# Optimization experiments

Measured on AMD Instinct MI355X. Metric: run time of the kernel, lower is better.

Reference implementation:

```python
import jax, jax.numpy as jnp
import numpy as np

F = 1024      # features
CF = 768      # context_features
H = 8         # num_heads
D = 64        # head_features
MID = H * D   # 512
SCALE = D ** -0.5


def _ln(x, g, b):
    m = jnp.mean(x, axis=-1, keepdims=True)
    v = jnp.var(x, axis=-1, keepdims=True)
    return (x - m) / jnp.sqrt(v + 1e-5) * g + b


def _attention(x, ctx, ng, nb, ncg, ncb, wq, wkv, wo, bo):
    # pre-norms (Attention.forward)
    xn = _ln(x, ng, nb)
    cn = _ln(ctx, ncg, ncb)
    q = xn @ wq                              # [b, n, MID]
    k, v = jnp.split(cn @ wkv, 2, axis=-1)   # [b, m, MID] each
    b, n, _ = q.shape
    m = k.shape[1]
    q = q.reshape(b, n, H, D).transpose(0, 2, 1, 3)  # b h n d
    k = k.reshape(b, m, H, D).transpose(0, 2, 1, 3)
    v = v.reshape(b, m, H, D).transpose(0, 2, 1, 3)
    sim = jnp.einsum('bhnd,bhmd->bhnm', q, k) * SCALE   # use_rel_pos=False
    attn = jax.nn.softmax(sim, axis=-1)
    out = jnp.einsum('bhnm,bhmd->bhnd', attn, v)
    out = out.transpose(0, 2, 1, 3).reshape(b, n, MID)
    return out @ wo + bo


def setup_inputs() -> dict:
    key = jax.random.key(0)
    ks = jax.random.split(key, 16)
    s = 0.02
    inp = {
        'x': jax.random.normal(ks[0], (4, 2048, F), jnp.float32),
        'context': jax.random.normal(ks[1], (4, 512, CF), jnp.float32),
        # self-attention params
        'sa_ng': jnp.ones((F,), jnp.float32),
        'sa_nb': jnp.zeros((F,), jnp.float32),
        'sa_ncg': jnp.ones((F,), jnp.float32),
        'sa_ncb': jnp.zeros((F,), jnp.float32),
        'sa_wq': jax.random.normal(ks[2], (F, MID), jnp.float32) * s,
        'sa_wkv': jax.random.normal(ks[3], (F, 2 * MID), jnp.float32) * s,
        'sa_wo': jax.random.normal(ks[4], (MID, F), jnp.float32) * s,
        'sa_bo': jnp.zeros((F,), jnp.float32),
        # cross-attention params
        'ca_ng': jnp.ones((F,), jnp.float32),
        'ca_nb': jnp.zeros((F,), jnp.float32),
        'ca_ncg': jnp.ones((CF,), jnp.float32),
        'ca_ncb': jnp.zeros((CF,), jnp.float32),
        'ca_wq': jax.random.normal(ks[5], (F, MID), jnp.float32) * s,
        'ca_wkv': jax.random.normal(ks[6], (CF, 2 * MID), jnp.float32) * s,
        'ca_wo': jax.random.normal(ks[7], (MID, F), jnp.float32) * s,
        'ca_bo': jnp.zeros((F,), jnp.float32),
    }
    return inp


def reference(x, context,
              sa_ng, sa_nb, sa_ncg, sa_ncb, sa_wq, sa_wkv, sa_wo, sa_bo,
              ca_ng, ca_nb, ca_ncg, ca_ncb, ca_wq, ca_wkv, ca_wo, ca_bo):
    # AttentionBlock.forward: x = self_attn(x) + x; x = cross_attn(x, ctx) + x
    x = _attention(x, x, sa_ng, sa_nb, sa_ncg, sa_ncb, sa_wq, sa_wkv, sa_wo, sa_bo) + x
    x = _attention(x, context, ca_ng, ca_nb, ca_ncg, ca_ncb, ca_wq, ca_wkv, ca_wo, ca_bo) + x
    return x
```

## Files before the change

kernel.cpp:

```cpp
#include <hip/hip_runtime.h>
#include <hip/hip_bf16.h>

typedef __bf16 bf16x8 __attribute__((ext_vector_type(8)));
typedef float  f32x4  __attribute__((ext_vector_type(4)));

#define MFMA16(a, b, c) __builtin_amdgcn_mfma_f32_16x16x32_bf16((a), (b), (c), 0, 0, 0)

__device__ __forceinline__ void async16(void* lds, const void* g) {
    __builtin_amdgcn_global_load_lds(
        (const __attribute__((address_space(1))) unsigned int*)g,
        (__attribute__((address_space(3))) unsigned int*)lds, 16, 0, 0);
}

__global__ __launch_bounds__(256) void tconv_kernel(const float* __restrict__ W,
                                                    __bf16* __restrict__ WT,
                                                    int K, int N) {
    __shared__ __bf16 t[64][65];
    int n0 = blockIdx.x * 64, k0 = blockIdx.y * 64;
    int tx = threadIdx.x & 63, ty = threadIdx.x >> 6;
    for (int r = ty; r < 64; r += 4)
        t[r][tx] = (__bf16)W[(size_t)(k0 + r) * N + n0 + tx];
    __syncthreads();
    for (int rr = ty; rr < 64; rr += 4)
        WT[(size_t)(n0 + rr) * K + k0 + tx] = t[tx][rr];
}

template <int C>
__global__ __launch_bounds__(256) void ln_kernel(const float* __restrict__ x,
                                                 const float* __restrict__ g,
                                                 const float* __restrict__ b,
                                                 __bf16* __restrict__ out) {
    int row = blockIdx.x;
    const float* xr = x + (size_t)row * C;
    float s1 = 0.f, s2 = 0.f;
    float v[(C == 1024) ? 4 : 3];
    if constexpr (C == 1024) {
        float4 f = *(const float4*)&xr[threadIdx.x * 4];
        v[0] = f.x; v[1] = f.y; v[2] = f.z; v[3] = f.w;
#pragma unroll
        for (int i = 0; i < 4; i++) { s1 += v[i]; s2 += v[i] * v[i]; }
    } else {
#pragma unroll
        for (int i = 0; i < 3; i++) {
            v[i] = xr[threadIdx.x + i * 256];
            s1 += v[i]; s2 += v[i] * v[i];
        }
    }
#pragma unroll
    for (int off = 1; off < 64; off <<= 1) {
        s1 += __shfl_xor(s1, off);
        s2 += __shfl_xor(s2, off);
    }
    __shared__ float p1[4], p2[4];
    int wave = threadIdx.x >> 6;
    if ((threadIdx.x & 63) == 0) { p1[wave] = s1; p2[wave] = s2; }
    __syncthreads();
    s1 = p1[0] + p1[1] + p1[2] + p1[3];
    s2 = p2[0] + p2[1] + p2[2] + p2[3];
    float mean = s1 / C;
    float rstd = rsqrtf(s2 / C - mean * mean + 1e-5f);
    __bf16* orow = out + (size_t)row * C;
    if constexpr (C == 1024) {
        union { __bf16 h[4]; unsigned long long u; } pk;
#pragma unroll
        for (int i = 0; i < 4; i++) {
            int c = threadIdx.x * 4 + i;
            pk.h[i] = (__bf16)((v[i] - mean) * rstd * g[c] + b[c]);
        }
        *(unsigned long long*)&orow[threadIdx.x * 4] = pk.u;
    } else {
#pragma unroll
        for (int i = 0; i < 3; i++) {
            int c = threadIdx.x + i * 256;
            orow[c] = (__bf16)((v[i] - mean) * rstd * g[c] + b[c]);
        }
    }
}

__global__ __launch_bounds__(256) void ln2_kernel(const float* __restrict__ x,
                                                  const float* __restrict__ g1,
                                                  const float* __restrict__ b1,
                                                  const float* __restrict__ g2,
                                                  const float* __restrict__ b2,
                                                  __bf16* __restrict__ o1,
                                                  __bf16* __restrict__ o2) {
    constexpr int C = 1024;
    int row = blockIdx.x;
    const float* xr = x + (size_t)row * C;
    float4 f = *(const float4*)&xr[threadIdx.x * 4];
    float v[4] = {f.x, f.y, f.z, f.w};
    float s1 = 0.f, s2 = 0.f;
#pragma unroll
    for (int i = 0; i < 4; i++) { s1 += v[i]; s2 += v[i] * v[i]; }
#pragma unroll
    for (int off = 1; off < 64; off <<= 1) {
        s1 += __shfl_xor(s1, off);
        s2 += __shfl_xor(s2, off);
    }
    __shared__ float p1[4], p2[4];
    int wave = threadIdx.x >> 6;
    if ((threadIdx.x & 63) == 0) { p1[wave] = s1; p2[wave] = s2; }
    __syncthreads();
    s1 = p1[0] + p1[1] + p1[2] + p1[3];
    s2 = p2[0] + p2[1] + p2[2] + p2[3];
    float mean = s1 / C;
    float rstd = rsqrtf(s2 / C - mean * mean + 1e-5f);
    union { __bf16 h[4]; unsigned long long u; } pk1, pk2;
#pragma unroll
    for (int i = 0; i < 4; i++) {
        int c = threadIdx.x * 4 + i;
        float nv = (v[i] - mean) * rstd;
        pk1.h[i] = (__bf16)(nv * g1[c] + b1[c]);
        pk2.h[i] = (__bf16)(nv * g2[c] + b2[c]);
    }
    *(unsigned long long*)&o1[(size_t)row * C + threadIdx.x * 4] = pk1.u;
    *(unsigned long long*)&o2[(size_t)row * C + threadIdx.x * 4] = pk2.u;
}

template <int EPI>
__device__ __forceinline__ void gemm_core(const __bf16* __restrict__ A,
                                          const __bf16* __restrict__ BT,
                                          void* __restrict__ Cout,
                                          int N, int K, int bm, int bn,
                                          const float* __restrict__ bias,
                                          const float* __restrict__ res,
                                          __bf16* Al, __bf16* Bl) {
    int tid = threadIdx.x;
    int lane = tid & 63, wave = tid >> 6;
    int quad = lane >> 4, l15 = lane & 15;
    int wm = wave >> 1, wn = wave & 1;
    const __bf16* Ab = A + (size_t)(bm * 128) * K;
    const __bf16* Bb = BT + (size_t)(bn * 128) * K;
    f32x4 acc[4][4] = {};
    for (int k0 = 0; k0 < K; k0 += 32) {
#pragma unroll
        for (int j = 0; j < 2; j++) {
            int sbase = wave * 128 + j * 64;
            int s = sbase + lane;
            int r = s >> 2, c = (s & 3) ^ (r & 3);
            async16((char*)Al + sbase * 16, &Ab[(size_t)r * K + k0 + c * 8]);
            async16((char*)Bl + sbase * 16, &Bb[(size_t)r * K + k0 + c * 8]);
        }
        __syncthreads();
        bf16x8 a[4], b[4];
#pragma unroll
        for (int i = 0; i < 4; i++) {
            int row = wm * 64 + i * 16 + l15;
            a[i] = *(const bf16x8*)&Al[row * 32 + (quad ^ (row & 3)) * 8];
        }
#pragma unroll
        for (int t = 0; t < 4; t++) {
            int row = wn * 64 + t * 16 + l15;
            b[t] = *(const bf16x8*)&Bl[row * 32 + (quad ^ (row & 3)) * 8];
        }
#pragma unroll
        for (int i = 0; i < 4; i++)
#pragma unroll
            for (int t = 0; t < 4; t++) acc[i][t] = MFMA16(a[i], b[t], acc[i][t]);
        __syncthreads();
    }
#pragma unroll
    for (int i = 0; i < 4; i++) {
#pragma unroll
        for (int t = 0; t < 4; t++) {
#pragma unroll
            for (int r = 0; r < 4; r++) {
                int row = bm * 128 + wm * 64 + i * 16 + quad * 4 + r;
                int col = bn * 128 + wn * 64 + t * 16 + l15;
                float vv = acc[i][t][r];
                if (EPI == 0) {
                    ((__bf16*)Cout)[(size_t)row * N + col] = (__bf16)vv;
                } else {
                    ((float*)Cout)[(size_t)row * N + col] =
                        vv + bias[col] + res[(size_t)row * N + col];
                }
            }
        }
    }
}

template <int EPI>
__global__ __launch_bounds__(256) void gemm_bt(const __bf16* __restrict__ A,
                                               const __bf16* __restrict__ BT,
                                               void* __restrict__ Cout,
                                               int M, int N, int K,
                                               const float* __restrict__ bias,
                                               const float* __restrict__ res) {
    __shared__ __align__(16) __bf16 Al[128 * 32];
    __shared__ __align__(16) __bf16 Bl[128 * 32];
    gemm_core<EPI>(A, BT, Cout, N, K, blockIdx.x, blockIdx.y, bias, res, Al, Bl);
}

__global__ __launch_bounds__(256) void gemm_fused3(
    const __bf16* A0, const __bf16* B0, __bf16* C0, int N0, int K0, int nbn0,
    const __bf16* A1, const __bf16* B1, __bf16* C1, int N1, int K1, int nbn1,
    const __bf16* A2, const __bf16* B2, __bf16* C2, int N2, int K2, int nbn2,
    int c0, int c1) {
    __shared__ __align__(16) __bf16 Al[128 * 32];
    __shared__ __align__(16) __bf16 Bl[128 * 32];
    int id = blockIdx.x;
    if (id < c0) {
        gemm_core<0>(A0, B0, C0, N0, K0, id / nbn0, id % nbn0, nullptr, nullptr, Al, Bl);
    } else if (id < c1) {
        id -= c0;
        gemm_core<0>(A1, B1, C1, N1, K1, id / nbn1, id % nbn1, nullptr, nullptr, Al, Bl);
    } else {
        id -= c1;
        gemm_core<0>(A2, B2, C2, N2, K2, id / nbn2, id % nbn2, nullptr, nullptr, Al, Bl);
    }
}

__global__ __launch_bounds__(256) void flash_kernel(const __bf16* __restrict__ q,
                                                    const __bf16* __restrict__ kb,
                                                    const __bf16* __restrict__ vt,
                                                    __bf16* __restrict__ out,
                                                    int n, int m) {
    __shared__ __align__(16) __bf16 Qs[64 * 64];
    __shared__ __align__(16) __bf16 Ks[64 * 64];
    __shared__ __align__(16) __bf16 VTs[64 * 64];
    __shared__ __align__(16) __bf16 Ps[64 * 64];
    int tid = threadIdx.x;
    int lane = tid & 63, w = tid >> 6;
    int quad = lane >> 4, l15 = lane & 15;
    int qt = blockIdx.x, h = blockIdx.y, b = blockIdx.z;
    const size_t BM = (size_t)gridDim.z * m;
    const int qrow = w * 16 + l15;

#pragma unroll
    for (int j = 0; j < 2; j++) {
        int sbase = w * 128 + j * 64;
        int s = sbase + lane;
        int r = s >> 3, c = (s & 7) ^ (r & 7);
        async16((char*)Qs + sbase * 16,
                &q[(size_t)(b * n + qt * 64 + r) * 512 + h * 64 + c * 8]);
    }

    f32x4 acc[4] = {};
    float l_part = 0.f;

    int nkt = m / 64;
    for (int kt = 0; kt < nkt; kt++) {
#pragma unroll
        for (int j = 0; j < 2; j++) {
            int sbase = w * 128 + j * 64;
            int s = sbase + lane;
            int r = s >> 3, c = (s & 7) ^ (r & 7);
            async16((char*)Ks + sbase * 16,
                    &kb[(size_t)(b * m + kt * 64 + r) * 512 + h * 64 + c * 8]);
            async16((char*)VTs + sbase * 16,
                    &vt[(size_t)(h * 64 + r) * BM + b * m + kt * 64 + c * 8]);
        }
        __syncthreads();

        f32x4 sacc[4] = {};
#pragma unroll
        for (int kk = 0; kk < 64; kk += 32) {
            int jb = ((kk >> 3) + quad) ^ (qrow & 7);
            bf16x8 bq = *(const bf16x8*)&Qs[qrow * 64 + jb * 8];
#pragma unroll
            for (int t = 0; t < 4; t++) {
                int krow = t * 16 + l15;
                int ja = ((kk >> 3) + quad) ^ (krow & 7);
                bf16x8 ak = *(const bf16x8*)&Ks[krow * 64 + ja * 8];
                sacc[t] = MFMA16(ak, bq, sacc[t]);
            }
        }

#pragma unroll
        for (int t = 0; t < 4; t++) {
            float e0 = __expf(sacc[t][0] * 0.125f);
            float e1 = __expf(sacc[t][1] * 0.125f);
            float e2 = __expf(sacc[t][2] * 0.125f);
            float e3 = __expf(sacc[t][3] * 0.125f);
            l_part += (e0 + e1) + (e2 + e3);
            union { __bf16 h[4]; unsigned long long u; } pk;
            pk.h[0] = (__bf16)e0; pk.h[1] = (__bf16)e1;
            pk.h[2] = (__bf16)e2; pk.h[3] = (__bf16)e3;
            int chunk = t * 2 + (quad >> 1);
            int off = qrow * 64 + (chunk ^ (qrow & 7)) * 8 + (quad & 1) * 4;
            *(unsigned long long*)&Ps[off] = pk.u;
        }

#pragma unroll
        for (int kk = 0; kk < 64; kk += 32) {
            int jp = ((kk >> 3) + quad) ^ (qrow & 7);
            bf16x8 ap = *(const bf16x8*)&Ps[qrow * 64 + jp * 8];
#pragma unroll
            for (int t2 = 0; t2 < 4; t2++) {
                int drow = t2 * 16 + l15;
                int jv = ((kk >> 3) + quad) ^ (drow & 7);
                bf16x8 bv = *(const bf16x8*)&VTs[drow * 64 + jv * 8];
                acc[t2] = MFMA16(ap, bv, acc[t2]);
            }
        }
        __syncthreads();
    }

    l_part += __shfl_xor(l_part, 16);
    l_part += __shfl_xor(l_part, 32);
    float rinv = 1.0f / l_part;
#pragma unroll
    for (int r = 0; r < 4; r++) {
        float rl = __shfl(rinv, quad * 4 + r);
        int row = b * n + qt * 64 + w * 16 + quad * 4 + r;
#pragma unroll
        for (int t2 = 0; t2 < 4; t2++)
            out[(size_t)row * 512 + h * 64 + t2 * 16 + l15] =
                (__bf16)(acc[t2][r] * rl);
    }
}

extern "C" void kernel_launch(void* const* d_in, const int* in_sizes, int n_in,
                              void* d_out, int out_size, void* d_ws, size_t ws_size,
                              hipStream_t stream) {
    const float* x      = (const float*)d_in[0];
    const float* ctx    = (const float*)d_in[1];
    const float* sa_ng  = (const float*)d_in[2];
    const float* sa_nb  = (const float*)d_in[3];
    const float* sa_ncg = (const float*)d_in[4];
    const float* sa_ncb = (const float*)d_in[5];
    const float* sa_wq  = (const float*)d_in[6];
    const float* sa_wkv = (const float*)d_in[7];
    const float* sa_wo  = (const float*)d_in[8];
    const float* sa_bo  = (const float*)d_in[9];
    const float* ca_ng  = (const float*)d_in[10];
    const float* ca_nb  = (const float*)d_in[11];
    const float* ca_ncg = (const float*)d_in[12];
    const float* ca_ncb = (const float*)d_in[13];
    const float* ca_wq  = (const float*)d_in[14];
    const float* ca_wkv = (const float*)d_in[15];
    const float* ca_wo  = (const float*)d_in[16];
    const float* ca_bo  = (const float*)d_in[17];
    float* out = (float*)d_out;

    const int B = 4, N = 2048, M = 512, F = 1024, CF = 768, MID = 512;
    const int ROWS = B * N;
    const int CROWS = B * M;

    char* ws = (char*)d_ws;
    size_t off = 0;
    auto alloc = [&](size_t bytes) {
        void* p = ws + off;
        off = (off + bytes + 255) & ~(size_t)255;
        return p;
    };
    __bf16* wqT   = (__bf16*)alloc((size_t)MID * F * 2);
    __bf16* wkvT  = (__bf16*)alloc((size_t)(2 * MID) * F * 2);
    __bf16* woT   = (__bf16*)alloc((size_t)F * MID * 2);
    __bf16* cwqT  = (__bf16*)alloc((size_t)MID * F * 2);
    __bf16* cwkvT = (__bf16*)alloc((size_t)(2 * MID) * CF * 2);
    __bf16* cwoT  = (__bf16*)alloc((size_t)F * MID * 2);
    __bf16* xn1   = (__bf16*)alloc((size_t)ROWS * F * 2);
    __bf16* xn2   = (__bf16*)alloc((size_t)ROWS * F * 2);
    __bf16* qb    = (__bf16*)alloc((size_t)ROWS * MID * 2);
    __bf16* kb    = (__bf16*)alloc((size_t)ROWS * MID * 2);
    __bf16* vt    = (__bf16*)alloc((size_t)MID * ROWS * 2);
    __bf16* ao    = (__bf16*)alloc((size_t)ROWS * MID * 2);
    float*  x1    = (float*)alloc((size_t)ROWS * F * 4);
    (void)ws_size; (void)in_sizes; (void)n_in; (void)out_size;

    dim3 blk(256);

    tconv_kernel<<<dim3(MID / 64, F / 64), blk, 0, stream>>>(sa_wq, wqT, F, MID);
    tconv_kernel<<<dim3((2 * MID) / 64, F / 64), blk, 0, stream>>>(sa_wkv, wkvT, F, 2 * MID);
    tconv_kernel<<<dim3(F / 64, MID / 64), blk, 0, stream>>>(sa_wo, woT, MID, F);
    tconv_kernel<<<dim3(MID / 64, F / 64), blk, 0, stream>>>(ca_wq, cwqT, F, MID);
    tconv_kernel<<<dim3((2 * MID) / 64, CF / 64), blk, 0, stream>>>(ca_wkv, cwkvT, CF, 2 * MID);
    tconv_kernel<<<dim3(F / 64, MID / 64), blk, 0, stream>>>(ca_wo, cwoT, MID, F);

    ln2_kernel<<<dim3(ROWS), blk, 0, stream>>>(x, sa_ng, sa_nb, sa_ncg, sa_ncb, xn1, xn2);
    {
        int c0 = (ROWS / 128) * (MID / 128);
        int c1 = c0 + (ROWS / 128) * (MID / 128);
        int c2 = c1 + (MID / 128) * (ROWS / 128);
        gemm_fused3<<<dim3(c2), blk, 0, stream>>>(
            xn1, wqT, qb, MID, F, MID / 128,
            xn2, wkvT, kb, MID, F, MID / 128,
            wkvT + (size_t)MID * F, xn2, vt, ROWS, F, ROWS / 128,
            c0, c1);
    }
    flash_kernel<<<dim3(N / 64, 8, B), blk, 0, stream>>>(qb, kb, vt, ao, N, N);
    gemm_bt<1><<<dim3(ROWS / 128, F / 128), blk, 0, stream>>>(
        ao, woT, x1, ROWS, F, MID, sa_bo, x);

    ln_kernel<1024><<<dim3(ROWS), blk, 0, stream>>>(x1, ca_ng, ca_nb, xn1);
    ln_kernel<768><<<dim3(CROWS), blk, 0, stream>>>(ctx, ca_ncg, ca_ncb, xn2);
    {
        int c0 = (ROWS / 128) * (MID / 128);
        int c1 = c0 + (CROWS / 128) * (MID / 128);
        int c2 = c1 + (MID / 128) * (CROWS / 128);
        gemm_fused3<<<dim3(c2), blk, 0, stream>>>(
            xn1, cwqT, qb, MID, F, MID / 128,
            xn2, cwkvT, kb, MID, CF, MID / 128,
            cwkvT + (size_t)MID * CF, xn2, vt, CROWS, CF, CROWS / 128,
            c0, c1);
    }
    flash_kernel<<<dim3(N / 64, 8, B), blk, 0, stream>>>(qb, kb, vt, ao, N, M);
    gemm_bt<1><<<dim3(ROWS / 128, F / 128), blk, 0, stream>>>(
        ao, cwoT, out, ROWS, F, MID, ca_bo, x1);
}
```

Baseline: 355.4 us.

## Merge weight-transpose and LN launches, widen GEMM K-tile, fold softmax scale into Q

Merges the six weight-transpose launches into one kernel, and the two cross-attention layernorm launches into one. Doubles the GEMM K step to 64 with an 8-way XOR swizzle, halving the number of barrier pairs per tile. Folds the softmax scale and log2(e) into the Q projection epilogue so the flash kernel can use a raw exp2 builtin instead of a scaled expf. Rounding Q to bf16 after scaling changes numerics slightly, and the larger LDS tiles may lower occupancy.

```diff
diff --git a/kernel.cpp b/kernel.cpp
--- a/kernel.cpp
+++ b/kernel.cpp
@@ -5,6 +5,14 @@
 typedef float  f32x4  __attribute__((ext_vector_type(4)));
 
 #define MFMA16(a, b, c) __builtin_amdgcn_mfma_f32_16x16x32_bf16((a), (b), (c), 0, 0, 0)
+
+__device__ __forceinline__ float fast_exp2(float x) {
+#if __has_builtin(__builtin_amdgcn_exp2f)
+    return __builtin_amdgcn_exp2f(x);
+#else
+    return exp2f(x);
+#endif
+}
 
 __device__ __forceinline__ void async16(void* lds, const void* g) {
     __builtin_amdgcn_global_load_lds(
@@ -12,28 +20,43 @@
         (__attribute__((address_space(3))) unsigned int*)lds, 16, 0, 0);
 }
 
-__global__ __launch_bounds__(256) void tconv_kernel(const float* __restrict__ W,
-                                                    __bf16* __restrict__ WT,
-                                                    int K, int N) {
-    __shared__ __bf16 t[64][65];
-    int n0 = blockIdx.x * 64, k0 = blockIdx.y * 64;
+__device__ __forceinline__ void tconv_tile(const float* __restrict__ W,
+                                           __bf16* __restrict__ WT,
+                                           int K, int N, int id, int nbx,
+                                           __bf16 (*t)[65]) {
+    int n0 = (id % nbx) * 64, k0 = (id / nbx) * 64;
     int tx = threadIdx.x & 63, ty = threadIdx.x >> 6;
+#pragma unroll
     for (int r = ty; r < 64; r += 4)
         t[r][tx] = (__bf16)W[(size_t)(k0 + r) * N + n0 + tx];
     __syncthreads();
+#pragma unroll
     for (int rr = ty; rr < 64; rr += 4)
         WT[(size_t)(n0 + rr) * K + k0 + tx] = t[tx][rr];
 }
 
+__global__ __launch_bounds__(256) void tconv6_kernel(
+    const float* W0, __bf16* T0, const float* W1, __bf16* T1,
+    const float* W2, __bf16* T2, const float* W3, __bf16* T3,
+    const float* W4, __bf16* T4, const float* W5, __bf16* T5) {
+    __shared__ __bf16 t[64][65];
+    int id = blockIdx.x;
+    if (id < 128)      tconv_tile(W0, T0, 1024, 512,  id,       8,  t);
+    else if (id < 384) tconv_tile(W1, T1, 1024, 1024, id - 128, 16, t);
+    else if (id < 512) tconv_tile(W2, T2, 512,  1024, id - 384, 16, t);
+    else if (id < 640) tconv_tile(W3, T3, 1024, 512,  id - 512, 8,  t);
+    else if (id < 832) tconv_tile(W4, T4, 768,  1024, id - 640, 16, t);
+    else               tconv_tile(W5, T5, 512,  1024, id - 832, 16, t);
+}
+
 template <int C>
-__global__ __launch_bounds__(256) void ln_kernel(const float* __restrict__ x,
-                                                 const float* __restrict__ g,
-                                                 const float* __restrict__ b,
-                                                 __bf16* __restrict__ out) {
-    int row = blockIdx.x;
-    const float* xr = x + (size_t)row * C;
-    float s1 = 0.f, s2 = 0.f;
-    float v[(C == 1024) ? 4 : 3];
+__device__ __forceinline__ void ln_body(const float* __restrict__ xr,
+                                        const float* __restrict__ g,
+                                        const float* __restrict__ b,
+                                        __bf16* __restrict__ orow,
+                                        float* p1, float* p2) {
+    constexpr int NP = (C == 1024) ? 4 : 3;
+    float v[NP], s1 = 0.f, s2 = 0.f;
     if constexpr (C == 1024) {
         float4 f = *(const float4*)&xr[threadIdx.x * 4];
         v[0] = f.x; v[1] = f.y; v[2] = f.z; v[3] = f.w;
@@ -51,7 +74,6 @@
         s1 += __shfl_xor(s1, off);
         s2 += __shfl_xor(s2, off);
     }
-    __shared__ float p1[4], p2[4];
     int wave = threadIdx.x >> 6;
     if ((threadIdx.x & 63) == 0) { p1[wave] = s1; p2[wave] = s2; }
     __syncthreads();
@@ -59,7 +81,6 @@
     s2 = p2[0] + p2[1] + p2[2] + p2[3];
     float mean = s1 / C;
     float rstd = rsqrtf(s2 / C - mean * mean + 1e-5f);
-    __bf16* orow = out + (size_t)row * C;
     if constexpr (C == 1024) {
         union { __bf16 h[4]; unsigned long long u; } pk;
 #pragma unroll
@@ -117,6 +138,21 @@
     *(unsigned long long*)&o2[(size_t)row * C + threadIdx.x * 4] = pk2.u;
 }
 
+__global__ __launch_bounds__(256) void ln_cross_kernel(
+    const float* __restrict__ x1, const float* __restrict__ g1, const float* __restrict__ b1,
+    __bf16* __restrict__ o1,
+    const float* __restrict__ ctx, const float* __restrict__ g2, const float* __restrict__ b2,
+    __bf16* __restrict__ o2, int rows1) {
+    __shared__ float p1[4], p2[4];
+    int id = blockIdx.x;
+    if (id < rows1) {
+        ln_body<1024>(x1 + (size_t)id * 1024, g1, b1, o1 + (size_t)id * 1024, p1, p2);
+    } else {
+        int row = id - rows1;
+        ln_body<768>(ctx + (size_t)row * 768, g2, b2, o2 + (size_t)row * 768, p1, p2);
+    }
+}
+
 template <int EPI>
 __device__ __forceinline__ void gemm_core(const __bf16* __restrict__ A,
                                           const __bf16* __restrict__ BT,
@@ -124,6 +160,7 @@
                                           int N, int K, int bm, int bn,
                                           const float* __restrict__ bias,
                                           const float* __restrict__ res,
+                                          float scale,
                                           __bf16* Al, __bf16* Bl) {
     int tid = threadIdx.x;
     int lane = tid & 63, wave = tid >> 6;
@@ -132,31 +169,34 @@
     const __bf16* Ab = A + (size_t)(bm * 128) * K;
     const __bf16* Bb = BT + (size_t)(bn * 128) * K;
     f32x4 acc[4][4] = {};
-    for (int k0 = 0; k0 < K; k0 += 32) {
-#pragma unroll
-        for (int j = 0; j < 2; j++) {
-            int sbase = wave * 128 + j * 64;
+    for (int k0 = 0; k0 < K; k0 += 64) {
+#pragma unroll
+        for (int j = 0; j < 4; j++) {
+            int sbase = wave * 256 + j * 64;
             int s = sbase + lane;
-            int r = s >> 2, c = (s & 3) ^ (r & 3);
+            int r = s >> 3, c = (s & 7) ^ (r & 7);
             async16((char*)Al + sbase * 16, &Ab[(size_t)r * K + k0 + c * 8]);
             async16((char*)Bl + sbase * 16, &Bb[(size_t)r * K + k0 + c * 8]);
         }
         __syncthreads();
-        bf16x8 a[4], b[4];
-#pragma unroll
-        for (int i = 0; i < 4; i++) {
-            int row = wm * 64 + i * 16 + l15;
-            a[i] = *(const bf16x8*)&Al[row * 32 + (quad ^ (row & 3)) * 8];
-        }
-#pragma unroll
-        for (int t = 0; t < 4; t++) {
-            int row = wn * 64 + t * 16 + l15;
-            b[t] = *(const bf16x8*)&Bl[row * 32 + (quad ^ (row & 3)) * 8];
-        }
-#pragma unroll
-        for (int i = 0; i < 4; i++)
-#pragma unroll
-            for (int t = 0; t < 4; t++) acc[i][t] = MFMA16(a[i], b[t], acc[i][t]);
+#pragma unroll
+        for (int ks = 0; ks < 2; ks++) {
+            bf16x8 a[4], b[4];
+#pragma unroll
+            for (int i = 0; i < 4; i++) {
+                int row = wm * 64 + i * 16 + l15;
+                a[i] = *(const bf16x8*)&Al[row * 64 + ((ks * 4 + quad) ^ (row & 7)) * 8];
+            }
+#pragma unroll
+            for (int t = 0; t < 4; t++) {
+                int row = wn * 64 + t * 16 + l15;
+                b[t] = *(const bf16x8*)&Bl[row * 64 + ((ks * 4 + quad) ^ (row & 7)) * 8];
+            }
+#pragma unroll
+            for (int i = 0; i < 4; i++)
+#pragma unroll
+                for (int t = 0; t < 4; t++) acc[i][t] = MFMA16(a[i], b[t], acc[i][t]);
+        }
         __syncthreads();
     }
 #pragma unroll
@@ -169,7 +209,7 @@
                 int col = bn * 128 + wn * 64 + t * 16 + l15;
                 float vv = acc[i][t][r];
                 if (EPI == 0) {
-                    ((__bf16*)Cout)[(size_t)row * N + col] = (__bf16)vv;
+                    ((__bf16*)Cout)[(size_t)row * N + col] = (__bf16)(vv * scale);
                 } else {
                     ((float*)Cout)[(size_t)row * N + col] =
                         vv + bias[col] + res[(size_t)row * N + col];
@@ -186,27 +226,27 @@
                                                int M, int N, int K,
                                                const float* __restrict__ bias,
                                                const float* __restrict__ res) {
-    __shared__ __align__(16) __bf16 Al[128 * 32];
-    __shared__ __align__(16) __bf16 Bl[128 * 32];
-    gemm_core<EPI>(A, BT, Cout, N, K, blockIdx.x, blockIdx.y, bias, res, Al, Bl);
+    __shared__ __align__(16) __bf16 Al[128 * 64];
+    __shared__ __align__(16) __bf16 Bl[128 * 64];
+    gemm_core<EPI>(A, BT, Cout, N, K, blockIdx.x, blockIdx.y, bias, res, 1.0f, Al, Bl);
 }
 
 __global__ __launch_bounds__(256) void gemm_fused3(
-    const __bf16* A0, const __bf16* B0, __bf16* C0, int N0, int K0, int nbn0,
-    const __bf16* A1, const __bf16* B1, __bf16* C1, int N1, int K1, int nbn1,
-    const __bf16* A2, const __bf16* B2, __bf16* C2, int N2, int K2, int nbn2,
+    const __bf16* A0, const __bf16* B0, __bf16* C0, int N0, int K0, int nbn0, float sc0,
+    const __bf16* A1, const __bf16* B1, __bf16* C1, int N1, int K1, int nbn1, float sc1,
+    const __bf16* A2, const __bf16* B2, __bf16* C2, int N2, int K2, int nbn2, float sc2,
     int c0, int c1) {
-    __shared__ __align__(16) __bf16 Al[128 * 32];
-    __shared__ __align__(16) __bf16 Bl[128 * 32];
+    __shared__ __align__(16) __bf16 Al[128 * 64];
+    __shared__ __align__(16) __bf16 Bl[128 * 64];
     int id = blockIdx.x;
     if (id < c0) {
-        gemm_core<0>(A0, B0, C0, N0, K0, id / nbn0, id % nbn0, nullptr, nullptr, Al, Bl);
+        gemm_core<0>(A0, B0, C0, N0, K0, id / nbn0, id % nbn0, nullptr, nullptr, sc0, Al, Bl);
     } else if (id < c1) {
         id -= c0;
-        gemm_core<0>(A1, B1, C1, N1, K1, id / nbn1, id % nbn1, nullptr, nullptr, Al, Bl);
+        gemm_core<0>(A1, B1, C1, N1, K1, id / nbn1, id % nbn1, nullptr, nullptr, sc1, Al, Bl);
     } else {
         id -= c1;
-        gemm_core<0>(A2, B2, C2, N2, K2, id / nbn2, id % nbn2, nullptr, nullptr, Al, Bl);
+        gemm_core<0>(A2, B2, C2, N2, K2, id / nbn2, id % nbn2, nullptr, nullptr, sc2, Al, Bl);
     }
 }
 
@@ -268,10 +308,10 @@
 
 #pragma unroll
         for (int t = 0; t < 4; t++) {
-            float e0 = __expf(sacc[t][0] * 0.125f);
-            float e1 = __expf(sacc[t][1] * 0.125f);
-            float e2 = __expf(sacc[t][2] * 0.125f);
-            float e3 = __expf(sacc[t][3] * 0.125f);
+            float e0 = fast_exp2(sacc[t][0]);
+            float e1 = fast_exp2(sacc[t][1]);
+            float e2 = fast_exp2(sacc[t][2]);
+            float e3 = fast_exp2(sacc[t][3]);
             l_part += (e0 + e1) + (e2 + e3);
             union { __bf16 h[4]; unsigned long long u; } pk;
             pk.h[0] = (__bf16)e0; pk.h[1] = (__bf16)e1;
@@ -336,6 +376,7 @@
     const int B = 4, N = 2048, M = 512, F = 1024, CF = 768, MID = 512;
     const int ROWS = B * N;
     const int CROWS = B * M;
+    const float QSCALE = 0.125f * 1.4426950408889634f;
 
     char* ws = (char*)d_ws;
     size_t off = 0;
@@ -361,12 +402,8 @@
 
     dim3 blk(256);
 
-    tconv_kernel<<<dim3(MID / 64, F / 64), blk, 0, stream>>>(sa_wq, wqT, F, MID);
-    tconv_kernel<<<dim3((2 * MID) / 64, F / 64), blk, 0, stream>>>(sa_wkv, wkvT, F, 2 * MID);
-    tconv_kernel<<<dim3(F / 64, MID / 64), blk, 0, stream>>>(sa_wo, woT, MID, F);
-    tconv_kernel<<<dim3(MID / 64, F / 64), blk, 0, stream>>>(ca_wq, cwqT, F, MID);
-    tconv_kernel<<<dim3((2 * MID) / 64, CF / 64), blk, 0, stream>>>(ca_wkv, cwkvT, CF, 2 * MID);
-    tconv_kernel<<<dim3(F / 64, MID / 64), blk, 0, stream>>>(ca_wo, cwoT, MID, F);
+    tconv6_kernel<<<dim3(960), blk, 0, stream>>>(
+        sa_wq, wqT, sa_wkv, wkvT, sa_wo, woT, ca_wq, cwqT, ca_wkv, cwkvT, ca_wo, cwoT);
 
     ln2_kernel<<<dim3(ROWS), blk, 0, stream>>>(x, sa_ng, sa_nb, sa_ncg, sa_ncb, xn1, xn2);
     {
@@ -374,25 +411,25 @@
         int c1 = c0 + (ROWS / 128) * (MID / 128);
         int c2 = c1 + (MID / 128) * (ROWS / 128);
         gemm_fused3<<<dim3(c2), blk, 0, stream>>>(
-            xn1, wqT, qb, MID, F, MID / 128,
-            xn2, wkvT, kb, MID, F, MID / 128,
-            wkvT + (size_t)MID * F, xn2, vt, ROWS, F, ROWS / 128,
+            xn1, wqT, qb, MID, F, MID / 128, QSCALE,
+            xn2, wkvT, kb, MID, F, MID / 128, 1.0f,
+            wkvT + (size_t)MID * F, xn2, vt, ROWS, F, ROWS / 128, 1.0f,
             c0, c1);
     }
     flash_kernel<<<dim3(N / 64, 8, B), blk, 0, stream>>>(qb, kb, vt, ao, N, N);
     gemm_bt<1><<<dim3(ROWS / 128, F / 128), blk, 0, stream>>>(
         ao, woT, x1, ROWS, F, MID, sa_bo, x);
 
-    ln_kernel<1024><<<dim3(ROWS), blk, 0, stream>>>(x1, ca_ng, ca_nb, xn1);
-    ln_kernel<768><<<dim3(CROWS), blk, 0, stream>>>(ctx, ca_ncg, ca_ncb, xn2);
+    ln_cross_kernel<<<dim3(ROWS + CROWS), blk, 0, stream>>>(
+        x1, ca_ng, ca_nb, xn1, ctx, ca_ncg, ca_ncb, xn2, ROWS);
     {
         int c0 = (ROWS / 128) * (MID / 128);
         int c1 = c0 + (CROWS / 128) * (MID / 128);
         int c2 = c1 + (MID / 128) * (CROWS / 128);
         gemm_fused3<<<dim3(c2), blk, 0, stream>>>(
-            xn1, cwqT, qb, MID, F, MID / 128,
-            xn2, cwkvT, kb, MID, CF, MID / 128,
-            cwkvT + (size_t)MID * CF, xn2, vt, CROWS, CF, CROWS / 128,
+            xn1, cwqT, qb, MID, F, MID / 128, QSCALE,
+            xn2, cwkvT, kb, MID, CF, MID / 128, 1.0f,
+            cwkvT + (size_t)MID * CF, xn2, vt, CROWS, CF, CROWS / 128, 1.0f,
             c0, c1);
     }
     flash_kernel<<<dim3(N / 64, 8, B), blk, 0, stream>>>(qb, kb, vt, ao, N, M);
```

Result: faster. 314.8 us (-11.4%).
